# Kernel optimization log

Measured on AMD Instinct MI355X. Metric: run time of the kernel, lower is better.

The kernel has to match this reference:

```python
import jax, jax.numpy as jnp
import numpy as np
import math

B, C, H, W = 16, 256, 96, 96
S = 3  # num_stages
OUT_C = 64


def _pos_encoding(c, h, w):
    # Faithful vectorization of generate_fixed_cosine_positional_encoding.
    pos_y = jnp.linspace(0.0, 1.0, h)
    pos_x = jnp.linspace(0.0, 1.0, w)
    py, px = jnp.meshgrid(pos_y, pos_x, indexing='ij')  # [H, W]
    i_vals = np.arange(0, c // 2, 2)                    # loop indices i
    freqs = jnp.exp(jnp.asarray(i_vals, jnp.float32) * -(math.log(10000.0) / (c // 2)))  # div_term[i//2]
    sin_part = jnp.sin(px[None] * freqs[:, None, None]) + jnp.sin(py[None] * freqs[:, None, None])
    cos_part = jnp.cos(px[None] * freqs[:, None, None]) + jnp.cos(py[None] * freqs[:, None, None])
    pe = jnp.zeros((c, h, w), jnp.float32)
    pe = pe.at[2 * i_vals].set(sin_part).at[2 * i_vals + 1].set(cos_part)
    return pe


def _nearest_resize(wmap, h, w):
    # torch F.interpolate(mode='nearest'): src_idx = floor(dst_idx * in/out)
    hw, ww = wmap.shape[-2], wmap.shape[-1]
    ih = (jnp.arange(h) * hw) // h
    iw = (jnp.arange(w) * ww) // w
    return wmap[..., ih[:, None], iw[None, :]]


def _conv1x1(x, w, b):
    return jnp.einsum('oc,bchw->bohw', w, x) + b[None, :, None, None]


def setup_inputs():
    key = jax.random.key(0)
    ks = jax.random.split(key, 12)
    sc = 0.3 / math.sqrt(C)
    return {
        'x1': jax.random.normal(ks[0], (B, C, H, W), jnp.float32),
        'x2': jax.random.normal(ks[1], (B, C, H, W), jnp.float32),
        'weight_vis': jax.random.uniform(ks[2], (B, H, W), jnp.float32),
        'weight_ir': jax.random.uniform(ks[3], (B, H, W), jnp.float32),
        'q_w': jax.random.normal(ks[4], (S, C, C), jnp.float32) * sc,
        'q_b': jnp.zeros((S, C), jnp.float32),
        'k_w': jax.random.normal(ks[5], (S, C, C), jnp.float32) * sc,
        'k_b': jnp.zeros((S, C), jnp.float32),
        'v_w': jax.random.normal(ks[6], (S, C, C), jnp.float32) * sc,
        'v_b': jnp.zeros((S, C), jnp.float32),
        'proj_w': jax.random.normal(ks[7], (OUT_C, C), jnp.float32) * sc,
        'proj_b': jnp.zeros((OUT_C,), jnp.float32),
    }


def reference(x1, x2, weight_vis, weight_ir, q_w, q_b, k_w, k_b, v_w, v_b, proj_w, proj_b):
    pe = _pos_encoding(x1.shape[1], x1.shape[2], x1.shape[3])  # combined_pos_encoding = pe1
    h, w = x1.shape[2], x1.shape[3]
    w_vis = _nearest_resize(weight_vis[:, None], h, w)  # [B,1,H,W]
    w_ir = _nearest_resize(weight_ir[:, None], h, w)
    fused = x1
    for i in range(S):
        x1 = x1 * w_vis
        x2 = x2 * w_ir
        q = _conv1x1(x1, q_w[i], q_b[i]) + pe[None]          # [B,C,H,W]
        k = _conv1x1(x2, k_w[i], k_b[i]) + pe[None]
        v = _conv1x1(x2, v_w[i], v_b[i])
        logits = jnp.einsum('bchw,bcgw->bchg', q, k)         # per-channel QK^T: [B,C,H,H]
        attn = jax.nn.softmax(logits, axis=-1)
        fused = jnp.einsum('bchg,bcgw->bchw', attn, v)       # [B,C,H,W]
        x1, x2 = fused, fused
    return _conv1x1(fused, proj_w, proj_b)                    # [B,64,H,W]
```

## Files before the change

### kernel.cpp

```cpp
#include <hip/hip_runtime.h>
#include <hip/hip_bf16.h>
#include <math.h>

#define NPOS 9216
#define PERB 2359296ull

typedef unsigned short u16;
typedef __attribute__((ext_vector_type(8))) short short8;
typedef __attribute__((ext_vector_type(4))) float f32x4;

__device__ inline u16 bfhi(float x) {
    unsigned int b = __float_as_uint(x);
    return (u16)((b + 0x7FFFu + ((b >> 16) & 1u)) >> 16);
}
__device__ inline float bf2f(u16 u) { return __uint_as_float(((unsigned int)u) << 16); }

typedef const __attribute__((address_space(1))) void* gvp;
typedef __attribute__((address_space(3))) void* lvp;
__device__ __forceinline__ void glds16(const void* g, void* l) {
    __builtin_amdgcn_global_load_lds((gvp)g, (lvp)l, 16, 0, 0);
}

__global__ __launch_bounds__(256) void tt_kernel(float* __restrict__ T)
{
    int idx = blockIdx.x * 256 + threadIdx.x;
    int c = idx / 96, p = idx - (idx / 96) * 96;
    int j = c >> 2, r = c & 3;
    float f = expf(-(float)(2 * j) * 0.07195578415f);
    float x = (float)p * (1.0f / 95.0f) * f;
    T[idx] = (r == 0) ? sinf(x) : (r == 1) ? cosf(x) : 0.0f;
}

__global__ __launch_bounds__(256) void wsplit(
    const float* __restrict__ qw, const float* __restrict__ kw,
    const float* __restrict__ vw, u16* __restrict__ whi, u16* __restrict__ wlo)
{
    int bid = blockIdx.x;
    int s = bid / 48, rem = bid % 48;
    int mat = rem / 16, rem2 = rem % 16;
    int mb = rem2 / 8, kb = rem2 % 8;
    const float* W = ((mat == 0) ? qw : (mat == 1) ? kw : vw) + (size_t)s * 65536;
    int t = threadIdx.x;
    int m = t >> 1, kh = (t & 1) * 16;
    const float* src = W + (size_t)(mb * 128 + m) * 256 + kb * 32 + kh;
    int s0 = kh >> 3;
    int sw = (m >> 1) & 3;
    size_t ob = (size_t)s * 196608 + (size_t)((mat * 2 + mb) * 8 + kb) * 4096
              + (size_t)m * 32;
    u16 hv[16], lv[16];
#pragma unroll
    for (int j = 0; j < 16; ++j) {
        float x = src[j];
        u16 h = bfhi(x);
        hv[j] = h;
        lv[j] = bfhi(x - bf2f(h));
    }
    *(uint4*)(whi + ob + ((s0 ^ sw) * 8))       = *(uint4*)hv;
    *(uint4*)(whi + ob + (((s0 + 1) ^ sw) * 8)) = *(uint4*)(hv + 8);
    *(uint4*)(wlo + ob + ((s0 ^ sw) * 8))       = *(uint4*)lv;
    *(uint4*)(wlo + ob + (((s0 + 1) ^ sw) * 8)) = *(uint4*)(lv + 8);
}

__global__ __launch_bounds__(512, 4) void gemm_qkv_mfma(
    const u16* __restrict__ whi, const u16* __restrict__ wlo,
    const float* __restrict__ srcq, const float* __restrict__ srckv,
    const float* __restrict__ qb, const float* __restrict__ kbias,
    const float* __restrict__ vb, const float* __restrict__ wvis,
    const float* __restrict__ wir, const float* __restrict__ Ttab,
    float* __restrict__ qo, float* __restrict__ ko, float* __restrict__ vo)
{
    __shared__ char LDSBUF[49152];
    u16* AH = (u16*)LDSBUF;
    u16* AL = AH + 8192;
    u16* BH = AL + 8192;
    u16* BL = BH + 4096;

    int t = threadIdx.x;
    int d = blockIdx.x + 3 * blockIdx.y;
    int role = (d & 7) * 27 + (d >> 3);
    int mat = role / 72, bn = role % 72;
    int b = blockIdx.z;

    const float* gB = ((mat == 0) ? srcq : srckv) + (size_t)b * PERB + bn * 128;
    const u16* gA0 = whi + (size_t)(mat * 2) * 32768;
    const u16* gA1 = wlo + (size_t)(mat * 2) * 32768;

    int wv = t >> 6;
    int wm = wv >> 1, wn = wv & 1;
    int rr = t & 15, gq = (t >> 4) & 3;

    int sxor = (gq ^ ((rr >> 1) & 3)) * 8;
    int offA0 = (wm * 64 + rr) * 32 + sxor;
    int offB0 = (wn * 64 + rr) * 32 + sxor;

    int arow = t >> 2, acol = (t & 3) * 8;
    size_t asrc0 = (size_t)arow * 32 + acol;
    size_t asrc1 = 32768 + (size_t)arow * 32 + acol;

    int bn_ = t & 127, bkh = t >> 7;
    int key = (bn_ >> 1) & 3;
    int wrB = bn_ * 32 + ((bkh ^ key) * 8);
    const float* bp = gB + (size_t)(bkh * 8) * NPOS + bn_;

    f32x4 acc[4][4];
#pragma unroll
    for (int i = 0; i < 4; ++i)
#pragma unroll
        for (int j = 0; j < 4; ++j) acc[i][j] = (f32x4){0.f, 0.f, 0.f, 0.f};

    float xv[8];
#pragma unroll
    for (int j = 0; j < 8; ++j) xv[j] = bp[(size_t)j * NPOS];

    for (int kq = 0; kq < 8; ++kq) {
        {
            glds16(gA0 + kq * 4096 + asrc0, &AH[t * 8]);
            glds16(gA0 + kq * 4096 + asrc1, &AH[t * 8 + 4096]);
            glds16(gA1 + kq * 4096 + asrc0, &AL[t * 8]);
            glds16(gA1 + kq * 4096 + asrc1, &AL[t * 8 + 4096]);
        }
        {
            u16 hv[8], lv[8];
#pragma unroll
            for (int j = 0; j < 8; ++j) {
                float x = xv[j];
                u16 h = bfhi(x);
                hv[j] = h;
                lv[j] = bfhi(x - bf2f(h));
            }
            *(uint4*)(&BH[wrB]) = *(uint4*)hv;
            *(uint4*)(&BL[wrB]) = *(uint4*)lv;
        }
        __syncthreads();

        if (kq < 7) {
#pragma unroll
            for (int j = 0; j < 8; ++j)
                xv[j] = bp[(size_t)((kq + 1) * 32 + j) * NPOS];
        }

        short8 bh[4], bl[4];
#pragma unroll
        for (int r = 0; r < 4; ++r) {
            bh[r] = *(const short8*)(&BH[offB0 + r * 512]);
            bl[r] = *(const short8*)(&BL[offB0 + r * 512]);
        }
#pragma unroll
        for (int f = 0; f < 4; ++f) {
            short8 ah = *(const short8*)(&AH[offA0 + f * 512]);
            short8 al = *(const short8*)(&AL[offA0 + f * 512]);
#pragma unroll
            for (int r = 0; r < 4; ++r) {
                acc[f][r] = __builtin_amdgcn_mfma_f32_16x16x32_bf16(ah, bh[r], acc[f][r], 0, 0, 0);
                acc[f][r] = __builtin_amdgcn_mfma_f32_16x16x32_bf16(ah, bl[r], acc[f][r], 0, 0, 0);
                acc[f][r] = __builtin_amdgcn_mfma_f32_16x16x32_bf16(al, bh[r], acc[f][r], 0, 0, 0);
            }
        }
        asm volatile("s_waitcnt lgkmcnt(0)" ::: "memory");
        __builtin_amdgcn_s_barrier();
        __builtin_amdgcn_sched_barrier(0);
    }

    float* SB = (float*)LDSBUF + (size_t)wv * (16 * 68);
    const float* wmap = ((mat == 0) ? wvis : wir) + (size_t)b * NPOS;
    const float* bias = (mat == 0) ? qb : (mat == 1) ? kbias : vb;
    float* outp = ((mat == 0) ? qo : (mat == 1) ? ko : vo) + (size_t)b * PERB;
    bool addpe = (mat != 2);

    int lane = t & 63;
    int lrow = lane >> 2;
    int lq   = lane & 3;
    int base_n = bn * 128 + wn * 64;

#pragma unroll
    for (int f = 0; f < 4; ++f) {
#pragma unroll
        for (int r = 0; r < 4; ++r)
#pragma unroll
            for (int ri = 0; ri < 4; ++ri)
                SB[(gq * 4 + ri) * 68 + (r * 16 + rr)] = acc[f][r][ri];
        int o = wm * 64 + f * 16 + lrow;
        float bo = bias[o];
        const float* tro = Ttab + o * 96;
        float* orow = outp + (size_t)o * NPOS;
#pragma unroll
        for (int qd = 0; qd < 4; ++qd) {
            int c0 = lq * 16 + qd * 4;
            int n = base_n + c0;
            float4 v4 = *(float4*)&SB[lrow * 68 + c0];
            float4 s4 = *(const float4*)&wmap[n];
            float4 o4;
            if (addpe) {
                int hh = n / 96, ww = n - hh * 96;
                float4 pw4 = *(const float4*)&tro[ww];
                float ph = tro[hh];
                o4.x = v4.x * s4.x + bo + pw4.x + ph;
                o4.y = v4.y * s4.y + bo + pw4.y + ph;
                o4.z = v4.z * s4.z + bo + pw4.z + ph;
                o4.w = v4.w * s4.w + bo + pw4.w + ph;
            } else {
                o4.x = v4.x * s4.x + bo;
                o4.y = v4.y * s4.y + bo;
                o4.z = v4.z * s4.z + bo;
                o4.w = v4.w * s4.w + bo;
            }
            *(float4*)&orow[n] = o4;
        }
    }
}

__global__ __launch_bounds__(256) void attn_kernel(
    const float* __restrict__ q, const float* __restrict__ k,
    const float* __restrict__ v, float* __restrict__ fused)
{
    __shared__ float R1[96 * 102];
    __shared__ float R2[96 * 102];

    int t  = threadIdx.x;
    int bc = blockIdx.x;
    const size_t base = (size_t)bc * NPOS;

    for (int f = t; f < 96 * 24; f += 256) {
        int r = f / 24, w4 = (f % 24) * 4;
        *(float4*)(R1 + r * 102 + w4) = *(const float4*)(q + base + r * 96 + w4);
        *(float4*)(R2 + r * 102 + w4) = *(const float4*)(k + base + r * 96 + w4);
    }
    __syncthreads();

    int tx = t & 15, ty = t >> 4;
    int h0 = ty * 6, g0 = tx * 6;

    float acc[6][6];
#pragma unroll
    for (int i = 0; i < 6; ++i)
#pragma unroll
        for (int j = 0; j < 6; ++j) acc[i][j] = 0.0f;

    for (int w4 = 0; w4 < 24; ++w4) {
        float4 qv[6], kv[6];
#pragma unroll
        for (int i = 0; i < 6; ++i) qv[i] = *(const float4*)(R1 + (h0 + i) * 102 + w4 * 4);
#pragma unroll
        for (int j = 0; j < 6; ++j) kv[j] = *(const float4*)(R2 + (g0 + j) * 102 + w4 * 4);
#pragma unroll
        for (int i = 0; i < 6; ++i)
#pragma unroll
            for (int j = 0; j < 6; ++j) {
                acc[i][j] = fmaf(qv[i].x, kv[j].x, acc[i][j]);
                acc[i][j] = fmaf(qv[i].y, kv[j].y, acc[i][j]);
                acc[i][j] = fmaf(qv[i].z, kv[j].z, acc[i][j]);
                acc[i][j] = fmaf(qv[i].w, kv[j].w, acc[i][j]);
            }
    }

#pragma unroll
    for (int i = 0; i < 6; ++i) {
        float m = acc[i][0];
#pragma unroll
        for (int j = 1; j < 6; ++j) m = fmaxf(m, acc[i][j]);
        for (int d = 1; d < 16; d <<= 1) m = fmaxf(m, __shfl_xor(m, d));
        float s = 0.0f;
#pragma unroll
        for (int j = 0; j < 6; ++j) {
            acc[i][j] = __expf(acc[i][j] - m);
            s += acc[i][j];
        }
        for (int d = 1; d < 16; d <<= 1) s += __shfl_xor(s, d);
        float inv = 1.0f / s;
#pragma unroll
        for (int j = 0; j < 6; ++j) acc[i][j] *= inv;
    }

    __syncthreads();
#pragma unroll
    for (int i = 0; i < 6; ++i)
#pragma unroll
        for (int j = 0; j < 6; ++j) R1[(h0 + i) * 102 + g0 + j] = acc[i][j];
    for (int f = t; f < 96 * 24; f += 256) {
        int r = f / 24, w4 = (f % 24) * 4;
        *(float4*)(R2 + r * 102 + w4) = *(const float4*)(v + base + r * 96 + w4);
    }
    __syncthreads();

    int w0 = tx * 6;
    float outv[6][6];
#pragma unroll
    for (int i = 0; i < 6; ++i)
#pragma unroll
        for (int j = 0; j < 6; ++j) outv[i][j] = 0.0f;

    for (int g4 = 0; g4 < 24; ++g4) {
        float4 av[6];
#pragma unroll
        for (int i = 0; i < 6; ++i) av[i] = *(const float4*)(R1 + (h0 + i) * 102 + g4 * 4);
#pragma unroll
        for (int gg = 0; gg < 4; ++gg) {
            int g = g4 * 4 + gg;
            const float* vrow = R2 + g * 102 + w0;
            float2 v0 = *(const float2*)(vrow);
            float2 v1 = *(const float2*)(vrow + 2);
            float2 v2 = *(const float2*)(vrow + 4);
            float vr[6] = {v0.x, v0.y, v1.x, v1.y, v2.x, v2.y};
#pragma unroll
            for (int i = 0; i < 6; ++i) {
                float a = (gg == 0) ? av[i].x : (gg == 1) ? av[i].y : (gg == 2) ? av[i].z : av[i].w;
#pragma unroll
                for (int j = 0; j < 6; ++j) outv[i][j] = fmaf(a, vr[j], outv[i][j]);
            }
        }
    }

#pragma unroll
    for (int i = 0; i < 6; ++i) {
        float* op = fused + base + (size_t)(h0 + i) * 96 + w0;
#pragma unroll
        for (int j = 0; j < 6; ++j) op[j] = outv[i][j];
    }
}

__global__ __launch_bounds__(256) void proj_kernel(
    const float* __restrict__ fused, const float* __restrict__ pw,
    const float* __restrict__ pb, float* __restrict__ out)
{
    __shared__ float As[16 * 68];
    __shared__ float Bs[16 * 128];

    int t  = threadIdx.x;
    int n0 = blockIdx.x * 128;
    int b  = blockIdx.y;
    const float* B = fused + (size_t)b * PERB;
    int tx = t & 15, ty = t >> 4;

    float acc[4][8];
#pragma unroll
    for (int i = 0; i < 4; ++i)
#pragma unroll
        for (int j = 0; j < 8; ++j) acc[i][j] = 0.0f;

    for (int k0 = 0; k0 < 256; k0 += 16) {
        {
            int m = t >> 2, c4 = (t & 3) * 4;
            float4 av = *(const float4*)(pw + (size_t)m * 256 + k0 + c4);
            As[(c4 + 0) * 68 + m] = av.x;
            As[(c4 + 1) * 68 + m] = av.y;
            As[(c4 + 2) * 68 + m] = av.z;
            As[(c4 + 3) * 68 + m] = av.w;
        }
#pragma unroll
        for (int l = 0; l < 2; ++l) {
            int f = t + l * 256;
            int c = f >> 5, n4 = (f & 31) * 4;
            *(float4*)(Bs + c * 128 + n4) =
                *(const float4*)(B + (size_t)(k0 + c) * NPOS + n0 + n4);
        }
        __syncthreads();
#pragma unroll
        for (int kk = 0; kk < 16; ++kk) {
            float a[4], bb[8];
            *(float4*)(&a[0])  = *(const float4*)(As + kk * 68 + ty * 4);
            *(float4*)(&bb[0]) = *(const float4*)(Bs + kk * 128 + tx * 8);
            *(float4*)(&bb[4]) = *(const float4*)(Bs + kk * 128 + tx * 8 + 4);
#pragma unroll
            for (int i = 0; i < 4; ++i)
#pragma unroll
                for (int j = 0; j < 8; ++j)
                    acc[i][j] = fmaf(a[i], bb[j], acc[i][j]);
        }
        __syncthreads();
    }

    int n = n0 + tx * 8;
#pragma unroll
    for (int i = 0; i < 4; ++i) {
        int o = ty * 4 + i;
        float bias = pb[o];
        float vals[8];
#pragma unroll
        for (int j = 0; j < 8; ++j) vals[j] = acc[i][j] + bias;
        float* op = out + ((size_t)b * 64 + o) * NPOS + n;
        *(float4*)(op)     = *(float4*)(&vals[0]);
        *(float4*)(op + 4) = *(float4*)(&vals[4]);
    }
}

extern "C" void kernel_launch(void* const* d_in, const int* in_sizes, int n_in,
                              void* d_out, int out_size, void* d_ws, size_t ws_size,
                              hipStream_t stream)
{
    const float* x1   = (const float*)d_in[0];
    const float* x2   = (const float*)d_in[1];
    const float* wvis = (const float*)d_in[2];
    const float* wir  = (const float*)d_in[3];
    const float* qw   = (const float*)d_in[4];
    const float* qb   = (const float*)d_in[5];
    const float* kw   = (const float*)d_in[6];
    const float* kb   = (const float*)d_in[7];
    const float* vw   = (const float*)d_in[8];
    const float* vb   = (const float*)d_in[9];
    const float* pw   = (const float*)d_in[10];
    const float* pb   = (const float*)d_in[11];
    float* out = (float*)d_out;

    float* ws = (float*)d_ws;
    size_t F = ws_size / 4;
    size_t fixed = 350000;
    size_t avail = (F > fixed) ? (F - fixed) : 0;
    int G = (int)(avail / (4 * PERB));
    if (G < 1) G = 1;
    if (G > 8) G = 8;

    float* ttab  = ws;
    float* qbuf  = ws + 24576;
    float* kbuf  = qbuf + (size_t)G * PERB;
    float* vbuf  = kbuf + (size_t)G * PERB;
    float* fbuf  = vbuf + (size_t)G * PERB;
    u16*   whiP  = (u16*)(fbuf + (size_t)G * PERB);
    u16*   wloP  = whiP + 589824;

    tt_kernel<<<dim3(96), 256, 0, stream>>>(ttab);
    wsplit<<<dim3(144), 256, 0, stream>>>(qw, kw, vw, whiP, wloP);

    for (int b0 = 0; b0 < 16; b0 += G) {
        int g = (16 - b0 < G) ? (16 - b0) : G;
        for (int s = 0; s < 3; ++s) {
            const float* sq  = (s == 0) ? (x1 + (size_t)b0 * PERB) : fbuf;
            const float* skv = (s == 0) ? (x2 + (size_t)b0 * PERB) : fbuf;
            gemm_qkv_mfma<<<dim3(3, 72, g), 512, 0, stream>>>(
                whiP + (size_t)s * 196608, wloP + (size_t)s * 196608,
                sq, skv,
                qb + (size_t)s * 256, kb + (size_t)s * 256, vb + (size_t)s * 256,
                wvis + (size_t)b0 * NPOS, wir + (size_t)b0 * NPOS,
                ttab, qbuf, kbuf, vbuf);
            attn_kernel<<<dim3(256 * g), 256, 0, stream>>>(qbuf, kbuf, vbuf, fbuf);
        }
        proj_kernel<<<dim3(72, g), 256, 0, stream>>>(
            fbuf, pw, pb, out + (size_t)b0 * 64 * NPOS);
    }
}
```

Before: 1.903 ms.

## Move per-channel attention onto bf16 MFMA with hi/lo split precision

Replaces the scalar-FMA attention kernel with an MFMA version. Q, K, P and V are split into bf16 hi/lo pairs stored in swizzled LDS tiles, and both QK^T and PV run through 16x16x32 bf16 MFMA instructions (4 products for QK, 3 for PV) to approximate fp32 accuracy. Output is staged through LDS so global stores are coalesced. The block shrinks to 192 threads with 75 KB of LDS. This trades extra conversion work and a small accuracy loss for much higher matrix throughput.

```diff
diff --git a/kernel.cpp b/kernel.cpp
--- a/kernel.cpp
+++ b/kernel.cpp
@@ -209,112 +209,192 @@
     }
 }
 
-__global__ __launch_bounds__(256) void attn_kernel(
+__global__ __launch_bounds__(192, 2) void attn_mfma(
     const float* __restrict__ q, const float* __restrict__ k,
     const float* __restrict__ v, float* __restrict__ fused)
 {
-    __shared__ float R1[96 * 102];
-    __shared__ float R2[96 * 102];
-
-    int t  = threadIdx.x;
+    __shared__ char LB[76800];
+    u16* QH = (u16*)LB;
+    u16* QL = (u16*)(LB + 19200);
+    u16* KH = (u16*)(LB + 38400);
+    u16* KL = (u16*)(LB + 57600);
+    float* OB = (float*)LB;
+
+    int t = threadIdx.x;
     int bc = blockIdx.x;
-    const size_t base = (size_t)bc * NPOS;
-
-    for (int f = t; f < 96 * 24; f += 256) {
-        int r = f / 24, w4 = (f % 24) * 4;
-        *(float4*)(R1 + r * 102 + w4) = *(const float4*)(q + base + r * 96 + w4);
-        *(float4*)(R2 + r * 102 + w4) = *(const float4*)(k + base + r * 96 + w4);
+    size_t base = (size_t)bc * NPOS;
+    int wq = t >> 6, rr = t & 15, gq = (t >> 4) & 3;
+    int sxor = (gq ^ ((rr >> 1) & 3)) * 8;
+
+#pragma unroll
+    for (int i = 0; i < 12; ++i) {
+        int idx = i * 192 + t;
+        int row = idx / 24, c4 = (idx % 24) * 4;
+        int tile = c4 >> 5, kin = c4 & 31;
+        int a = tile * 3072 + row * 32 + (((kin >> 3) ^ ((row >> 1) & 3)) << 3) + (kin & 7);
+        float4 qv = *(const float4*)(q + base + row * 96 + c4);
+        float4 kv = *(const float4*)(k + base + row * 96 + c4);
+        unsigned int qh01, qh23, ql01, ql23, kh01, kh23, kl01, kl23;
+        {
+            u16 h0 = bfhi(qv.x), h1 = bfhi(qv.y), h2 = bfhi(qv.z), h3 = bfhi(qv.w);
+            u16 l0 = bfhi(qv.x - bf2f(h0)), l1 = bfhi(qv.y - bf2f(h1));
+            u16 l2 = bfhi(qv.z - bf2f(h2)), l3 = bfhi(qv.w - bf2f(h3));
+            qh01 = (unsigned)h0 | ((unsigned)h1 << 16); qh23 = (unsigned)h2 | ((unsigned)h3 << 16);
+            ql01 = (unsigned)l0 | ((unsigned)l1 << 16); ql23 = (unsigned)l2 | ((unsigned)l3 << 16);
+        }
+        {
+            u16 h0 = bfhi(kv.x), h1 = bfhi(kv.y), h2 = bfhi(kv.z), h3 = bfhi(kv.w);
+            u16 l0 = bfhi(kv.x - bf2f(h0)), l1 = bfhi(kv.y - bf2f(h1));
+            u16 l2 = bfhi(kv.z - bf2f(h2)), l3 = bfhi(kv.w - bf2f(h3));
+            kh01 = (unsigned)h0 | ((unsigned)h1 << 16); kh23 = (unsigned)h2 | ((unsigned)h3 << 16);
+            kl01 = (unsigned)l0 | ((unsigned)l1 << 16); kl23 = (unsigned)l2 | ((unsigned)l3 << 16);
+        }
+        *(uint2*)(QH + a) = (uint2){qh01, qh23};
+        *(uint2*)(QL + a) = (uint2){ql01, ql23};
+        *(uint2*)(KH + a) = (uint2){kh01, kh23};
+        *(uint2*)(KL + a) = (uint2){kl01, kl23};
     }
     __syncthreads();
 
-    int tx = t & 15, ty = t >> 4;
-    int h0 = ty * 6, g0 = tx * 6;
-
-    float acc[6][6];
-#pragma unroll
-    for (int i = 0; i < 6; ++i)
-#pragma unroll
-        for (int j = 0; j < 6; ++j) acc[i][j] = 0.0f;
-
-    for (int w4 = 0; w4 < 24; ++w4) {
-        float4 qv[6], kv[6];
-#pragma unroll
-        for (int i = 0; i < 6; ++i) qv[i] = *(const float4*)(R1 + (h0 + i) * 102 + w4 * 4);
-#pragma unroll
-        for (int j = 0; j < 6; ++j) kv[j] = *(const float4*)(R2 + (g0 + j) * 102 + w4 * 4);
-#pragma unroll
-        for (int i = 0; i < 6; ++i)
-#pragma unroll
-            for (int j = 0; j < 6; ++j) {
-                acc[i][j] = fmaf(qv[i].x, kv[j].x, acc[i][j]);
-                acc[i][j] = fmaf(qv[i].y, kv[j].y, acc[i][j]);
-                acc[i][j] = fmaf(qv[i].z, kv[j].z, acc[i][j]);
-                acc[i][j] = fmaf(qv[i].w, kv[j].w, acc[i][j]);
-            }
-    }
-
-#pragma unroll
-    for (int i = 0; i < 6; ++i) {
-        float m = acc[i][0];
-#pragma unroll
-        for (int j = 1; j < 6; ++j) m = fmaxf(m, acc[i][j]);
-        for (int d = 1; d < 16; d <<= 1) m = fmaxf(m, __shfl_xor(m, d));
-        float s = 0.0f;
-#pragma unroll
-        for (int j = 0; j < 6; ++j) {
-            acc[i][j] = __expf(acc[i][j] - m);
-            s += acc[i][j];
-        }
-        for (int d = 1; d < 16; d <<= 1) s += __shfl_xor(s, d);
-        float inv = 1.0f / s;
-#pragma unroll
-        for (int j = 0; j < 6; ++j) acc[i][j] *= inv;
-    }
+    f32x4 acc[2][6];
+#pragma unroll
+    for (int mt = 0; mt < 2; ++mt)
+#pragma unroll
+        for (int nt = 0; nt < 6; ++nt) acc[mt][nt] = (f32x4){0.f, 0.f, 0.f, 0.f};
+
+#pragma unroll
+    for (int ks = 0; ks < 3; ++ks) {
+        short8 qh2[2], ql2[2], kh6[6], kl6[6];
+#pragma unroll
+        for (int mt = 0; mt < 2; ++mt) {
+            int ra = ks * 3072 + (wq * 32 + mt * 16 + rr) * 32 + sxor;
+            qh2[mt] = *(const short8*)(QH + ra);
+            ql2[mt] = *(const short8*)(QL + ra);
+        }
+#pragma unroll
+        for (int nt = 0; nt < 6; ++nt) {
+            int rb = ks * 3072 + (nt * 16 + rr) * 32 + sxor;
+            kh6[nt] = *(const short8*)(KH + rb);
+            kl6[nt] = *(const short8*)(KL + rb);
+        }
+#pragma unroll
+        for (int mt = 0; mt < 2; ++mt)
+#pragma unroll
+            for (int nt = 0; nt < 6; ++nt) {
+                acc[mt][nt] = __builtin_amdgcn_mfma_f32_16x16x32_bf16(qh2[mt], kh6[nt], acc[mt][nt], 0, 0, 0);
+                acc[mt][nt] = __builtin_amdgcn_mfma_f32_16x16x32_bf16(qh2[mt], kl6[nt], acc[mt][nt], 0, 0, 0);
+                acc[mt][nt] = __builtin_amdgcn_mfma_f32_16x16x32_bf16(ql2[mt], kh6[nt], acc[mt][nt], 0, 0, 0);
+                acc[mt][nt] = __builtin_amdgcn_mfma_f32_16x16x32_bf16(ql2[mt], kl6[nt], acc[mt][nt], 0, 0, 0);
+            }
+    }
+
+#pragma unroll
+    for (int mt = 0; mt < 2; ++mt)
+#pragma unroll
+        for (int ri = 0; ri < 4; ++ri) {
+            float mx = acc[mt][0][ri];
+#pragma unroll
+            for (int nt = 1; nt < 6; ++nt) mx = fmaxf(mx, acc[mt][nt][ri]);
+            for (int dd = 1; dd < 16; dd <<= 1) mx = fmaxf(mx, __shfl_xor(mx, dd));
+            float s = 0.0f;
+#pragma unroll
+            for (int nt = 0; nt < 6; ++nt) {
+                float e = __expf(acc[mt][nt][ri] - mx);
+                acc[mt][nt][ri] = e;
+                s += e;
+            }
+            for (int dd = 1; dd < 16; dd <<= 1) s += __shfl_xor(s, dd);
+            float inv = 1.0f / s;
+#pragma unroll
+            for (int nt = 0; nt < 6; ++nt) acc[mt][nt][ri] *= inv;
+        }
 
     __syncthreads();
-#pragma unroll
-    for (int i = 0; i < 6; ++i)
-#pragma unroll
-        for (int j = 0; j < 6; ++j) R1[(h0 + i) * 102 + g0 + j] = acc[i][j];
-    for (int f = t; f < 96 * 24; f += 256) {
-        int r = f / 24, w4 = (f % 24) * 4;
-        *(float4*)(R2 + r * 102 + w4) = *(const float4*)(v + base + r * 96 + w4);
+
+#pragma unroll
+    for (int mt = 0; mt < 2; ++mt)
+#pragma unroll
+        for (int ri = 0; ri < 4; ++ri) {
+            int row = wq * 32 + mt * 16 + gq * 4 + ri;
+            int keyr = (row >> 1) & 3;
+#pragma unroll
+            for (int nt = 0; nt < 6; ++nt) {
+                float val = acc[mt][nt][ri];
+                u16 h = bfhi(val);
+                u16 l = bfhi(val - bf2f(h));
+                int slot = ((nt & 1) << 1) | (rr >> 3);
+                int a = (nt >> 1) * 3072 + row * 32 + ((slot ^ keyr) << 3) + (rr & 7);
+                QH[a] = h;
+                QL[a] = l;
+            }
+        }
+#pragma unroll
+    for (int i = 0; i < 12; ++i) {
+        int idx = i * 192 + t;
+        int grow = idx / 24, c4 = (idx % 24) * 4;
+        float4 vv = *(const float4*)(v + base + grow * 96 + c4);
+        int tile = grow >> 5, kin = grow & 31;
+        int slot = kin >> 3, off = kin & 7;
+#pragma unroll
+        for (int e = 0; e < 4; ++e) {
+            int w = c4 + e;
+            float val = (e == 0) ? vv.x : (e == 1) ? vv.y : (e == 2) ? vv.z : vv.w;
+            u16 h = bfhi(val);
+            u16 l = bfhi(val - bf2f(h));
+            int a = tile * 3072 + w * 32 + ((slot ^ ((w >> 1) & 3)) << 3) + off;
+            KH[a] = h;
+            KL[a] = l;
+        }
     }
     __syncthreads();
 
-    int w0 = tx * 6;
-    float outv[6][6];
-#pragma unroll
-    for (int i = 0; i < 6; ++i)
-#pragma unroll
-        for (int j = 0; j < 6; ++j) outv[i][j] = 0.0f;
-
-    for (int g4 = 0; g4 < 24; ++g4) {
-        float4 av[6];
-#pragma unroll
-        for (int i = 0; i < 6; ++i) av[i] = *(const float4*)(R1 + (h0 + i) * 102 + g4 * 4);
-#pragma unroll
-        for (int gg = 0; gg < 4; ++gg) {
-            int g = g4 * 4 + gg;
-            const float* vrow = R2 + g * 102 + w0;
-            float2 v0 = *(const float2*)(vrow);
-            float2 v1 = *(const float2*)(vrow + 2);
-            float2 v2 = *(const float2*)(vrow + 4);
-            float vr[6] = {v0.x, v0.y, v1.x, v1.y, v2.x, v2.y};
-#pragma unroll
-            for (int i = 0; i < 6; ++i) {
-                float a = (gg == 0) ? av[i].x : (gg == 1) ? av[i].y : (gg == 2) ? av[i].z : av[i].w;
-#pragma unroll
-                for (int j = 0; j < 6; ++j) outv[i][j] = fmaf(a, vr[j], outv[i][j]);
-            }
-        }
-    }
-
-#pragma unroll
-    for (int i = 0; i < 6; ++i) {
-        float* op = fused + base + (size_t)(h0 + i) * 96 + w0;
-#pragma unroll
-        for (int j = 0; j < 6; ++j) op[j] = outv[i][j];
+#pragma unroll
+    for (int mt = 0; mt < 2; ++mt)
+#pragma unroll
+        for (int nt = 0; nt < 6; ++nt) acc[mt][nt] = (f32x4){0.f, 0.f, 0.f, 0.f};
+
+#pragma unroll
+    for (int ks = 0; ks < 3; ++ks) {
+        short8 ph2[2], pl2[2], vh6[6], vl6[6];
+#pragma unroll
+        for (int mt = 0; mt < 2; ++mt) {
+            int ra = ks * 3072 + (wq * 32 + mt * 16 + rr) * 32 + sxor;
+            ph2[mt] = *(const short8*)(QH + ra);
+            pl2[mt] = *(const short8*)(QL + ra);
+        }
+#pragma unroll
+        for (int nt = 0; nt < 6; ++nt) {
+            int rb = ks * 3072 + (nt * 16 + rr) * 32 + sxor;
+            vh6[nt] = *(const short8*)(KH + rb);
+            vl6[nt] = *(const short8*)(KL + rb);
+        }
+#pragma unroll
+        for (int mt = 0; mt < 2; ++mt)
+#pragma unroll
+            for (int nt = 0; nt < 6; ++nt) {
+                acc[mt][nt] = __builtin_amdgcn_mfma_f32_16x16x32_bf16(ph2[mt], vh6[nt], acc[mt][nt], 0, 0, 0);
+                acc[mt][nt] = __builtin_amdgcn_mfma_f32_16x16x32_bf16(ph2[mt], vl6[nt], acc[mt][nt], 0, 0, 0);
+                acc[mt][nt] = __builtin_amdgcn_mfma_f32_16x16x32_bf16(pl2[mt], vh6[nt], acc[mt][nt], 0, 0, 0);
+            }
+    }
+    __syncthreads();
+
+#pragma unroll
+    for (int mt = 0; mt < 2; ++mt)
+#pragma unroll
+        for (int nt = 0; nt < 6; ++nt)
+#pragma unroll
+            for (int ri = 0; ri < 4; ++ri) {
+                int row = wq * 32 + mt * 16 + gq * 4 + ri;
+                OB[row * 100 + nt * 16 + rr] = acc[mt][nt][ri];
+            }
+    __syncthreads();
+#pragma unroll
+    for (int i = 0; i < 12; ++i) {
+        int idx = i * 192 + t;
+        int row = idx / 24, c4 = (idx % 24) * 4;
+        float4 o = *(const float4*)&OB[row * 100 + c4];
+        *(float4*)(fused + base + row * 96 + c4) = o;
     }
 }
 
@@ -431,7 +511,7 @@
                 qb + (size_t)s * 256, kb + (size_t)s * 256, vb + (size_t)s * 256,
                 wvis + (size_t)b0 * NPOS, wir + (size_t)b0 * NPOS,
                 ttab, qbuf, kbuf, vbuf);
-            attn_kernel<<<dim3(256 * g), 256, 0, stream>>>(qbuf, kbuf, vbuf, fbuf);
+            attn_mfma<<<dim3(256 * g), 192, 0, stream>>>(qbuf, kbuf, vbuf, fbuf);
         }
         proj_kernel<<<dim3(72, g), 256, 0, stream>>>(
             fbuf, pw, pb, out + (size_t)b0 * 64 * NPOS);
```

Result: faster. 1.575 ms (-17.2%).
